# Kernel tuning notes

Hardware: AMD Instinct MI355X
Metric: run time of the kernel (lower is better)

Reference implementation:

```python
import jax, jax.numpy as jnp
import numpy as np

D_MODEL = 512
N_HEADS = 8
HEAD_DIM = D_MODEL // N_HEADS


def setup_inputs() -> dict:
    key = jax.random.key(0)
    ks = jax.random.split(key, 9)
    B, S = 2, 2048
    s = 1.0 / np.sqrt(D_MODEL)
    return {
        "x": jax.random.normal(ks[0], (B, S, D_MODEL), dtype=jnp.float32),
        "wq": jax.random.uniform(ks[1], (D_MODEL, D_MODEL), jnp.float32, -s, s),
        "bq": jax.random.uniform(ks[2], (D_MODEL,), jnp.float32, -s, s),
        "wk": jax.random.uniform(ks[3], (D_MODEL, D_MODEL), jnp.float32, -s, s),
        "bk": jax.random.uniform(ks[4], (D_MODEL,), jnp.float32, -s, s),
        "wv": jax.random.uniform(ks[5], (D_MODEL, D_MODEL), jnp.float32, -s, s),
        "bv": jax.random.uniform(ks[6], (D_MODEL,), jnp.float32, -s, s),
        "wo": jax.random.uniform(ks[7], (D_MODEL, D_MODEL), jnp.float32, -s, s),
        "bo": jax.random.uniform(ks[8], (D_MODEL,), jnp.float32, -s, s),
    }


def reference(x, wq, bq, wk, bk, wv, bv, wo, bo):
    B, S, _ = x.shape
    # Linear layers (torch Linear: y = x @ W.T + b)
    q = x @ wq.T + bq
    k = x @ wk.T + bk
    v = x @ wv.T + bv
    # (B, H, S, Dh)
    def heads(t):
        return t.reshape(B, S, N_HEADS, HEAD_DIM).transpose(0, 2, 1, 3)
    q, k, v = heads(q), heads(k), heads(v)
    scale = 1.0 / np.sqrt(HEAD_DIM)
    scores = jnp.einsum("bhqd,bhkd->bhqk", q, k) * scale
    attn = jax.nn.softmax(scores, axis=-1)
    out = jnp.einsum("bhqk,bhkd->bhqd", attn, v)
    out = out.transpose(0, 2, 1, 3).reshape(B, S, D_MODEL)
    return out @ wo.T + bo
```

## Files before the change

kernel.cpp:

```cpp
#include <hip/hip_runtime.h>
#include <hip/hip_bf16.h>
#include <stdint.h>

typedef unsigned short u16;
typedef __attribute__((ext_vector_type(8))) short short8;
typedef __attribute__((ext_vector_type(4))) float f32x4;
typedef __attribute__((ext_vector_type(4))) unsigned int u32x4;

#define AS1 __attribute__((address_space(1)))
#define AS3 __attribute__((address_space(3)))

__device__ __forceinline__ u16 f2bf(float f) {
    uint32_t u = __float_as_uint(f);
    u += 0x7fffu + ((u >> 16) & 1u);
    return (u16)(u >> 16);
}

__device__ __forceinline__ uint32_t cvtpk(float a, float b) {
    uint32_t r;
    asm("v_cvt_pk_bf16_f32 %0, %1, %2" : "=v"(r) : "v"(a), "v"(b));
    return r;
}

__global__ __launch_bounds__(256) void cvt_kernel(
    const float* __restrict__ x, const float* __restrict__ wq,
    const float* __restrict__ wk, const float* __restrict__ wv,
    const float* __restrict__ wo, u16* __restrict__ dst)
{
    long e = ((long)blockIdx.x * 256 + threadIdx.x) * 8;
    const float* src; long off;
    if (e < 2097152L)      { src = x;  off = e; }
    else if (e < 2359296L) { src = wq; off = e - 2097152L; }
    else if (e < 2621440L) { src = wk; off = e - 2359296L; }
    else if (e < 2883584L) { src = wv; off = e - 2621440L; }
    else                   { src = wo; off = e - 2883584L; }
    float4 a = *(const float4*)(src + off);
    float4 b = *(const float4*)(src + off + 4);
    short8 v;
    v[0] = (short)f2bf(a.x); v[1] = (short)f2bf(a.y);
    v[2] = (short)f2bf(a.z); v[3] = (short)f2bf(a.w);
    v[4] = (short)f2bf(b.x); v[5] = (short)f2bf(b.y);
    v[6] = (short)f2bf(b.z); v[7] = (short)f2bf(b.w);
    *(short8*)(dst + e) = v;
}

__device__ __forceinline__ void gemm_core(
    const u16* __restrict__ A, const u16* __restrict__ Bm,
    int row0, int col0, u16* aSh, u16* bSh, int tid, f32x4 (&acc)[4][4])
{
    const int lane = tid & 63, w = tid >> 6;
    const int lg = lane >> 4, lj = lane & 15;
    const int wr = w >> 1, wc = w & 1;

    for (int ks = 0; ks < 8; ++ks) {
        const int k0 = ks * 64;
#pragma unroll
        for (int rd = 0; rd < 4; ++rd) {
            int t16 = rd * 256 + tid;
            int r = t16 >> 3, p = t16 & 7;
            int l = p ^ (r & 7);
            __builtin_amdgcn_global_load_lds(
                (const AS1 void*)(A + (size_t)(row0 + r) * 512 + k0 + l * 8),
                (AS3 void*)(aSh + t16 * 8), 16, 0, 0);
            __builtin_amdgcn_global_load_lds(
                (const AS1 void*)(Bm + (size_t)(col0 + r) * 512 + k0 + l * 8),
                (AS3 void*)(bSh + t16 * 8), 16, 0, 0);
        }
        __syncthreads();
#pragma unroll
        for (int kt = 0; kt < 2; ++kt) {
            short8 af[4], bf[4];
#pragma unroll
            for (int it = 0; it < 4; ++it) {
                int rowa = wr * 64 + it * 16 + lj;
                int c = kt * 4 + lg;
                af[it] = *(const short8*)((const char*)aSh + rowa * 128 + ((c ^ (rowa & 7)) << 4));
            }
#pragma unroll
            for (int jt = 0; jt < 4; ++jt) {
                int rowb = wc * 64 + jt * 16 + lj;
                int c = kt * 4 + lg;
                bf[jt] = *(const short8*)((const char*)bSh + rowb * 128 + ((c ^ (rowb & 7)) << 4));
            }
#pragma unroll
            for (int it = 0; it < 4; ++it)
#pragma unroll
                for (int jt = 0; jt < 4; ++jt)
                    acc[it][jt] = __builtin_amdgcn_mfma_f32_16x16x32_bf16(af[it], bf[jt], acc[it][jt], 0, 0, 0);
        }
        __syncthreads();
    }
}

__global__ __launch_bounds__(256) void gemm_qkv(
    const u16* __restrict__ xb, const u16* __restrict__ wqb, const u16* __restrict__ wvb,
    const float* __restrict__ bq, const float* __restrict__ bk, const float* __restrict__ bv,
    u16* __restrict__ Qb, u16* __restrict__ Kb, u16* __restrict__ Vtb)
{
    __shared__ u16 aSh[128 * 64];
    __shared__ u16 bSh[128 * 64];
    const int tid = threadIdx.x;
    const int lane = tid & 63, w = tid >> 6;
    const int lg = lane >> 4, lj = lane & 15;
    const int wr = w >> 1, wc = w & 1;
    const int id = blockIdx.x;

    f32x4 acc[4][4] = {};

    if (id < 256) {
        const int row0 = (id >> 3) * 128, col0 = (id & 7) * 128;
        gemm_core(xb, wqb, row0, col0, aSh, bSh, tid, acc);
#pragma unroll
        for (int jt = 0; jt < 4; ++jt) {
            int o = col0 + wc * 64 + jt * 16 + lj;
            float bias = (o < 512) ? bq[o] : bk[o - 512];
            float sc = (o < 512) ? 0.18033688011112042f : 1.0f;
            u16* base = (o < 512) ? Qb : Kb;
            int h = (o >> 6) & 7, d = o & 63;
#pragma unroll
            for (int it = 0; it < 4; ++it)
#pragma unroll
                for (int r = 0; r < 4; ++r) {
                    int n = row0 + wr * 64 + it * 16 + lg * 4 + r;
                    int b = n >> 11, s = n & 2047;
                    base[(size_t)(((b << 3) + h) * 2048 + s) * 64 + d] = f2bf((acc[it][jt][r] + bias) * sc);
                }
        }
    } else {
        const int idx = id - 256;
        const int row0 = (idx >> 5) * 128, col0 = (idx & 31) * 128;
        gemm_core(wvb, xb, row0, col0, aSh, bSh, tid, acc);
#pragma unroll
        for (int it = 0; it < 4; ++it)
#pragma unroll
            for (int r = 0; r < 4; ++r) {
                int orow = row0 + wr * 64 + it * 16 + lg * 4 + r;
                float bias = bv[orow];
#pragma unroll
                for (int jt = 0; jt < 4; ++jt) {
                    int n = col0 + wc * 64 + jt * 16 + lj;
                    Vtb[(size_t)orow * 4096 + n] = f2bf(acc[it][jt][r] + bias);
                }
            }
    }
}

__global__ __launch_bounds__(256) void gemm_out(
    const u16* __restrict__ A, const u16* __restrict__ Bm,
    const float* __restrict__ bias0, float* __restrict__ of32)
{
    __shared__ u16 aSh[128 * 64];
    __shared__ u16 bSh[128 * 64];
    const int tid = threadIdx.x;
    const int lane = tid & 63, w = tid >> 6;
    const int lg = lane >> 4, lj = lane & 15;
    const int wr = w >> 1, wc = w & 1;
    const int row0 = blockIdx.y * 128, col0 = blockIdx.x * 128;

    f32x4 acc[4][4] = {};
    gemm_core(A, Bm, row0, col0, aSh, bSh, tid, acc);

#pragma unroll
    for (int jt = 0; jt < 4; ++jt) {
        int o = col0 + wc * 64 + jt * 16 + lj;
        float bias = bias0[o];
#pragma unroll
        for (int it = 0; it < 4; ++it)
#pragma unroll
            for (int r = 0; r < 4; ++r) {
                int n = row0 + wr * 64 + it * 16 + lg * 4 + r;
                of32[(size_t)n * 512 + o] = acc[it][jt][r] + bias;
            }
    }
}

__global__ __launch_bounds__(256, 4) void attn_kernel(
    const u16* __restrict__ Qb, const u16* __restrict__ Kb,
    const u16* __restrict__ Vtb, float* __restrict__ accP, float* __restrict__ lP)
{
    __shared__ u16 kvSh[2][2][32 * 64];
    const int tid = threadIdx.x;
    const int lane = tid & 63, w = tid >> 6;
    const int lg = lane >> 4, lj = lane & 15;
    const int bh = blockIdx.x, b = bh >> 3, h = bh & 7;
    const int z = blockIdx.z;
    const u16* Qh = Qb + (size_t)bh * 2048 * 64;
    const u16* Kh = Kb + (size_t)bh * 2048 * 64;
    const u16* Vh = Vtb + (size_t)h * 64 * 4096 + b * 2048;
    const int q0 = blockIdx.y * 128 + w * 32;
    const int kvbase = z * 512;

    int koff[2][2];
#pragma unroll
    for (int kt = 0; kt < 2; ++kt)
#pragma unroll
        for (int jf = 0; jf < 2; ++jf) {
            int row = 8 * (lj >> 2) + 4 * jf + (lj & 3);
            int sk = (row & 3) ^ (((row >> 3) & 3) << 1);
            koff[kt][jf] = row * 128 + ((((kt * 4 + lg) ^ sk)) << 4);
        }
    int voff[4];
#pragma unroll
    for (int jd = 0; jd < 4; ++jd) {
        int row = jd * 16 + lj;
        voff[jd] = 4096 + row * 64 + ((lg ^ ((row >> 1) & 3)) << 4);
    }

    {
    }
    int r_ = tid >> 3, p_ = tid & 7;
    int sk_ = (r_ & 3) ^ (((r_ >> 3) & 3) << 1);
    const u16* Ks = Kh + (size_t)(kvbase + r_) * 64 + (p_ ^ sk_) * 8;
    int rv_ = tid >> 2, pv_ = tid & 3;
    const u16* Vs = Vh + (size_t)rv_ * 4096 + kvbase + (pv_ ^ ((rv_ >> 1) & 3)) * 8;
    u16* kd0 = kvSh[0][0] + tid * 8;
    u16* vd0 = kvSh[0][1] + tid * 8;

#define STAGE(KD, VD) do {                                                    \
    __builtin_amdgcn_global_load_lds((const AS1 void*)Ks, (AS3 void*)(KD), 16, 0, 0); \
    __builtin_amdgcn_global_load_lds((const AS1 void*)Vs, (AS3 void*)(VD), 16, 0, 0); \
    Ks += 2048; Vs += 32; } while (0)

    short8 qf[2][2];
#pragma unroll
    for (int g = 0; g < 2; ++g)
#pragma unroll
        for (int kt = 0; kt < 2; ++kt)
            qf[g][kt] = *(const short8*)(Qh + (size_t)(q0 + g * 16 + lj) * 64 + kt * 32 + lg * 8);

    const short8 vone = {0x3F80, 0x3F80, 0x3F80, 0x3F80, 0x3F80, 0x3F80, 0x3F80, 0x3F80};
    f32x4 accO[2][4] = {};
    f32x4 accO5[2] = {};

    auto COMPUTE = [&](int ofs) {
        const char* base = (const char*)kvSh + ofs;
        f32x4 sf[2][2] = {};
#pragma unroll
        for (int kt = 0; kt < 2; ++kt) {
            short8 kf0 = *(const short8*)(base + koff[kt][0]);
            short8 kf1 = *(const short8*)(base + koff[kt][1]);
            sf[0][0] = __builtin_amdgcn_mfma_f32_16x16x32_bf16(kf0, qf[0][kt], sf[0][0], 0, 0, 0);
            sf[0][1] = __builtin_amdgcn_mfma_f32_16x16x32_bf16(kf1, qf[0][kt], sf[0][1], 0, 0, 0);
            sf[1][0] = __builtin_amdgcn_mfma_f32_16x16x32_bf16(kf0, qf[1][kt], sf[1][0], 0, 0, 0);
            sf[1][1] = __builtin_amdgcn_mfma_f32_16x16x32_bf16(kf1, qf[1][kt], sf[1][1], 0, 0, 0);
        }
        u32x4 t0, t1;
        t0[0] = cvtpk(exp2f(sf[0][0][0]), exp2f(sf[0][0][1]));
        t0[1] = cvtpk(exp2f(sf[0][0][2]), exp2f(sf[0][0][3]));
        t0[2] = cvtpk(exp2f(sf[0][1][0]), exp2f(sf[0][1][1]));
        t0[3] = cvtpk(exp2f(sf[0][1][2]), exp2f(sf[0][1][3]));
        t1[0] = cvtpk(exp2f(sf[1][0][0]), exp2f(sf[1][0][1]));
        t1[1] = cvtpk(exp2f(sf[1][0][2]), exp2f(sf[1][0][3]));
        t1[2] = cvtpk(exp2f(sf[1][1][0]), exp2f(sf[1][1][1]));
        t1[3] = cvtpk(exp2f(sf[1][1][2]), exp2f(sf[1][1][3]));
        short8 pa0 = __builtin_bit_cast(short8, t0);
        short8 pa1 = __builtin_bit_cast(short8, t1);
        accO5[0] = __builtin_amdgcn_mfma_f32_16x16x32_bf16(pa0, vone, accO5[0], 0, 0, 0);
        accO5[1] = __builtin_amdgcn_mfma_f32_16x16x32_bf16(pa1, vone, accO5[1], 0, 0, 0);
#pragma unroll
        for (int jd = 0; jd < 4; ++jd) {
            short8 vf = *(const short8*)(base + voff[jd]);
            accO[0][jd] = __builtin_amdgcn_mfma_f32_16x16x32_bf16(pa0, vf, accO[0][jd], 0, 0, 0);
            accO[1][jd] = __builtin_amdgcn_mfma_f32_16x16x32_bf16(pa1, vf, accO[1][jd], 0, 0, 0);
        }
    };

    STAGE(kd0, vd0);
    __syncthreads();
    for (int it = 0; it < 8; ++it) {
        STAGE(kd0 + 4096, vd0 + 4096);
        COMPUTE(0);
        __syncthreads();
        if (it < 7) STAGE(kd0, vd0);
        COMPUTE(8192);
        __syncthreads();
    }
#undef STAGE

    float* accW = accP + (size_t)z * 2097152;
#pragma unroll
    for (int g = 0; g < 2; ++g)
#pragma unroll
        for (int r = 0; r < 4; ++r) {
            int q = q0 + g * 16 + lg * 4 + r;
            int s = b * 2048 + q;
#pragma unroll
            for (int jd = 0; jd < 4; ++jd)
                accW[(size_t)s * 512 + h * 64 + jd * 16 + lj] = accO[g][jd][r];
            if (lj == 0) lP[(z * 16 + bh) * 2048 + q] = accO5[g][r];
        }
}

__global__ __launch_bounds__(256) void combine_kernel(
    const float* __restrict__ accP, const float* __restrict__ lP, u16* __restrict__ Ob)
{
    int gid = blockIdx.x * 256 + threadIdx.x;
    int row = gid >> 6, cb = (gid & 63) * 8;
    int b = row >> 11, q = row & 2047;
    int h = (gid & 63) >> 3;
    int bh = b * 8 + h;
    float l = 0.0f;
#pragma unroll
    for (int z = 0; z < 4; ++z) l += lP[z * 32768 + bh * 2048 + q];
    float inv = 1.0f / l;
    float s[8] = {};
#pragma unroll
    for (int z = 0; z < 4; ++z) {
        const float* a = accP + (size_t)z * 2097152 + (size_t)row * 512 + cb;
        float4 x0 = *(const float4*)a, x1 = *(const float4*)(a + 4);
        s[0] += x0.x; s[1] += x0.y; s[2] += x0.z; s[3] += x0.w;
        s[4] += x1.x; s[5] += x1.y; s[6] += x1.z; s[7] += x1.w;
    }
    short8 o;
#pragma unroll
    for (int j = 0; j < 8; ++j) o[j] = (short)f2bf(s[j] * inv);
    *(short8*)(Ob + (size_t)gid * 8) = o;
}

extern "C" void kernel_launch(void* const* d_in, const int* in_sizes, int n_in,
                              void* d_out, int out_size, void* d_ws, size_t ws_size,
                              hipStream_t stream)
{
    const float* x  = (const float*)d_in[0];
    const float* wq = (const float*)d_in[1];
    const float* bq = (const float*)d_in[2];
    const float* wk = (const float*)d_in[3];
    const float* bk = (const float*)d_in[4];
    const float* wv = (const float*)d_in[5];
    const float* bv = (const float*)d_in[6];
    const float* wo = (const float*)d_in[7];
    const float* bo = (const float*)d_in[8];

    u16* w16 = (u16*)d_ws;
    u16* xb  = w16;
    u16* wqb = w16 + 2097152;
    u16* wvb = w16 + 2621440;
    u16* wob = w16 + 2883584;
    u16* Qb  = w16 + 3145728;
    u16* Kb  = w16 + 5242880;
    u16* Vtb = w16 + 7340032;
    u16* Ob  = w16 + 9437184;
    float* accPf = (float*)(w16 + 11534336);
    float* lPf   = accPf + 8388608;

    cvt_kernel<<<1536, 256, 0, stream>>>(x, wq, wk, wv, wo, w16);
    gemm_qkv<<<384, 256, 0, stream>>>(xb, wqb, wvb, bq, bk, bv, Qb, Kb, Vtb);
    attn_kernel<<<dim3(16, 16, 4), 256, 0, stream>>>(Qb, Kb, Vtb, accPf, lPf);
    combine_kernel<<<1024, 256, 0, stream>>>(accPf, lPf, Ob);
    gemm_out<<<dim3(4, 32), 256, 0, stream>>>(Ob, wob, bo, (float*)d_out);
}
```

Measured before the change: 72.72 us.

## Fuse split-KV combine into attention via last-block counter; use 128x64 GEMM tiles

Removes the separate combine kernel. Each attention block now increments a per-(head, query-tile) atomic counter, and the last of the four KV-split blocks reduces the partial accumulators and normalisers into bf16 output. The counter is zeroed inside the conversion kernel. The V projection and output projection GEMMs switch to a new 128x64 tile core, raising block counts from 128 to 256 for the output GEMM and from 128 to 256 for the V part, to fill more CUs. The trade-offs are extra atomics and thread fences, plus a serial reduction tail on the last-arriving blocks.

```diff
diff --git a/kernel.cpp b/kernel.cpp
--- a/kernel.cpp
+++ b/kernel.cpp
@@ -25,8 +25,9 @@
 __global__ __launch_bounds__(256) void cvt_kernel(
     const float* __restrict__ x, const float* __restrict__ wq,
     const float* __restrict__ wk, const float* __restrict__ wv,
-    const float* __restrict__ wo, u16* __restrict__ dst)
-{
+    const float* __restrict__ wo, u16* __restrict__ dst, int* __restrict__ cnt)
+{
+    if (blockIdx.x == 0) cnt[threadIdx.x] = 0;
     long e = ((long)blockIdx.x * 256 + threadIdx.x) * 8;
     const float* src; long off;
     if (e < 2097152L)      { src = x;  off = e; }
@@ -92,6 +93,60 @@
     }
 }
 
+__device__ __forceinline__ void gemm_core64(
+    const u16* __restrict__ A, const u16* __restrict__ Bm,
+    int row0, int col0, u16* aSh, u16* bSh, int tid, f32x4 (&acc)[4][2])
+{
+    const int lane = tid & 63, w = tid >> 6;
+    const int lg = lane >> 4, lj = lane & 15;
+    const int wr = w >> 1, wc = w & 1;
+
+    for (int ks = 0; ks < 8; ++ks) {
+        const int k0 = ks * 64;
+#pragma unroll
+        for (int rd = 0; rd < 4; ++rd) {
+            int t16 = rd * 256 + tid;
+            int r = t16 >> 3, p = t16 & 7;
+            int l = p ^ (r & 7);
+            __builtin_amdgcn_global_load_lds(
+                (const AS1 void*)(A + (size_t)(row0 + r) * 512 + k0 + l * 8),
+                (AS3 void*)(aSh + t16 * 8), 16, 0, 0);
+        }
+#pragma unroll
+        for (int rd = 0; rd < 2; ++rd) {
+            int t16 = rd * 256 + tid;
+            int r = t16 >> 3, p = t16 & 7;
+            int l = p ^ (r & 7);
+            __builtin_amdgcn_global_load_lds(
+                (const AS1 void*)(Bm + (size_t)(col0 + r) * 512 + k0 + l * 8),
+                (AS3 void*)(bSh + t16 * 8), 16, 0, 0);
+        }
+        __syncthreads();
+#pragma unroll
+        for (int kt = 0; kt < 2; ++kt) {
+            short8 af[4], bf[2];
+#pragma unroll
+            for (int it = 0; it < 4; ++it) {
+                int rowa = wr * 64 + it * 16 + lj;
+                int c = kt * 4 + lg;
+                af[it] = *(const short8*)((const char*)aSh + rowa * 128 + ((c ^ (rowa & 7)) << 4));
+            }
+#pragma unroll
+            for (int jt = 0; jt < 2; ++jt) {
+                int rowb = wc * 32 + jt * 16 + lj;
+                int c = kt * 4 + lg;
+                bf[jt] = *(const short8*)((const char*)bSh + rowb * 128 + ((c ^ (rowb & 7)) << 4));
+            }
+#pragma unroll
+            for (int it = 0; it < 4; ++it)
+#pragma unroll
+                for (int jt = 0; jt < 2; ++jt)
+                    acc[it][jt] = __builtin_amdgcn_mfma_f32_16x16x32_bf16(af[it], bf[jt], acc[it][jt], 0, 0, 0);
+        }
+        __syncthreads();
+    }
+}
+
 __global__ __launch_bounds__(256) void gemm_qkv(
     const u16* __restrict__ xb, const u16* __restrict__ wqb, const u16* __restrict__ wvb,
     const float* __restrict__ bq, const float* __restrict__ bk, const float* __restrict__ bv,
@@ -105,9 +160,8 @@
     const int wr = w >> 1, wc = w & 1;
     const int id = blockIdx.x;
 
-    f32x4 acc[4][4] = {};
-
     if (id < 256) {
+        f32x4 acc[4][4] = {};
         const int row0 = (id >> 3) * 128, col0 = (id & 7) * 128;
         gemm_core(xb, wqb, row0, col0, aSh, bSh, tid, acc);
 #pragma unroll
@@ -127,9 +181,10 @@
                 }
         }
     } else {
+        f32x4 acc[4][2] = {};
         const int idx = id - 256;
-        const int row0 = (idx >> 5) * 128, col0 = (idx & 31) * 128;
-        gemm_core(wvb, xb, row0, col0, aSh, bSh, tid, acc);
+        const int row0 = (idx >> 6) * 128, col0 = (idx & 63) * 64;
+        gemm_core64(wvb, xb, row0, col0, aSh, bSh, tid, acc);
 #pragma unroll
         for (int it = 0; it < 4; ++it)
 #pragma unroll
@@ -137,8 +192,8 @@
                 int orow = row0 + wr * 64 + it * 16 + lg * 4 + r;
                 float bias = bv[orow];
 #pragma unroll
-                for (int jt = 0; jt < 4; ++jt) {
-                    int n = col0 + wc * 64 + jt * 16 + lj;
+                for (int jt = 0; jt < 2; ++jt) {
+                    int n = col0 + wc * 32 + jt * 16 + lj;
                     Vtb[(size_t)orow * 4096 + n] = f2bf(acc[it][jt][r] + bias);
                 }
             }
@@ -150,19 +205,20 @@
     const float* __restrict__ bias0, float* __restrict__ of32)
 {
     __shared__ u16 aSh[128 * 64];
-    __shared__ u16 bSh[128 * 64];
+    __shared__ u16 bSh[64 * 64];
     const int tid = threadIdx.x;
     const int lane = tid & 63, w = tid >> 6;
     const int lg = lane >> 4, lj = lane & 15;
     const int wr = w >> 1, wc = w & 1;
-    const int row0 = blockIdx.y * 128, col0 = blockIdx.x * 128;
-
-    f32x4 acc[4][4] = {};
-    gemm_core(A, Bm, row0, col0, aSh, bSh, tid, acc);
-
-#pragma unroll
-    for (int jt = 0; jt < 4; ++jt) {
-        int o = col0 + wc * 64 + jt * 16 + lj;
+    const int id = blockIdx.x;
+    const int row0 = (id >> 3) * 128, col0 = (id & 7) * 64;
+
+    f32x4 acc[4][2] = {};
+    gemm_core64(A, Bm, row0, col0, aSh, bSh, tid, acc);
+
+#pragma unroll
+    for (int jt = 0; jt < 2; ++jt) {
+        int o = col0 + wc * 32 + jt * 16 + lj;
         float bias = bias0[o];
 #pragma unroll
         for (int it = 0; it < 4; ++it)
@@ -176,7 +232,8 @@
 
 __global__ __launch_bounds__(256, 4) void attn_kernel(
     const u16* __restrict__ Qb, const u16* __restrict__ Kb,
-    const u16* __restrict__ Vtb, float* __restrict__ accP, float* __restrict__ lP)
+    const u16* __restrict__ Vtb, float* __restrict__ accP, float* __restrict__ lP,
+    u16* __restrict__ Ob, int* __restrict__ cnt)
 {
     __shared__ u16 kvSh[2][2][32 * 64];
     const int tid = threadIdx.x;
@@ -206,8 +263,6 @@
         voff[jd] = 4096 + row * 64 + ((lg ^ ((row >> 1) & 3)) << 4);
     }
 
-    {
-    }
     int r_ = tid >> 3, p_ = tid & 7;
     int sk_ = (r_ & 3) ^ (((r_ >> 3) & 3) << 1);
     const u16* Ks = Kh + (size_t)(kvbase + r_) * 64 + (p_ ^ sk_) * 8;
@@ -289,32 +344,41 @@
                 accW[(size_t)s * 512 + h * 64 + jd * 16 + lj] = accO[g][jd][r];
             if (lj == 0) lP[(z * 16 + bh) * 2048 + q] = accO5[g][r];
         }
-}
-
-__global__ __launch_bounds__(256) void combine_kernel(
-    const float* __restrict__ accP, const float* __restrict__ lP, u16* __restrict__ Ob)
-{
-    int gid = blockIdx.x * 256 + threadIdx.x;
-    int row = gid >> 6, cb = (gid & 63) * 8;
-    int b = row >> 11, q = row & 2047;
-    int h = (gid & 63) >> 3;
-    int bh = b * 8 + h;
-    float l = 0.0f;
-#pragma unroll
-    for (int z = 0; z < 4; ++z) l += lP[z * 32768 + bh * 2048 + q];
-    float inv = 1.0f / l;
-    float s[8] = {};
-#pragma unroll
-    for (int z = 0; z < 4; ++z) {
-        const float* a = accP + (size_t)z * 2097152 + (size_t)row * 512 + cb;
-        float4 x0 = *(const float4*)a, x1 = *(const float4*)(a + 4);
-        s[0] += x0.x; s[1] += x0.y; s[2] += x0.z; s[3] += x0.w;
-        s[4] += x1.x; s[5] += x1.y; s[6] += x1.z; s[7] += x1.w;
-    }
-    short8 o;
-#pragma unroll
-    for (int j = 0; j < 8; ++j) o[j] = (short)f2bf(s[j] * inv);
-    *(short8*)(Ob + (size_t)gid * 8) = o;
+
+    __threadfence();
+    __shared__ int amLast;
+    if (tid == 0)
+        amLast = (atomicAdd(&cnt[bh * 16 + blockIdx.y], 1) == 3);
+    __syncthreads();
+    if (amLast) {
+        __threadfence();
+        int qi = tid >> 1, dh = (tid & 1) * 32;
+        int q = blockIdx.y * 128 + qi;
+        int s = b * 2048 + q;
+        float l = 0.0f;
+#pragma unroll
+        for (int zz = 0; zz < 4; ++zz) l += lP[(zz * 16 + bh) * 2048 + q];
+        float inv = 1.0f / l;
+        float sa[32] = {};
+#pragma unroll
+        for (int zz = 0; zz < 4; ++zz) {
+            const float* a = accP + (size_t)zz * 2097152 + (size_t)s * 512 + h * 64 + dh;
+#pragma unroll
+            for (int j = 0; j < 8; ++j) {
+                float4 v4 = *(const float4*)(a + j * 4);
+                sa[j * 4 + 0] += v4.x; sa[j * 4 + 1] += v4.y;
+                sa[j * 4 + 2] += v4.z; sa[j * 4 + 3] += v4.w;
+            }
+        }
+        u16* ob = Ob + (size_t)s * 512 + h * 64 + dh;
+#pragma unroll
+        for (int j = 0; j < 4; ++j) {
+            short8 o8;
+#pragma unroll
+            for (int k = 0; k < 8; ++k) o8[k] = (short)f2bf(sa[j * 8 + k] * inv);
+            *(short8*)(ob + j * 8) = o8;
+        }
+    }
 }
 
 extern "C" void kernel_launch(void* const* d_in, const int* in_sizes, int n_in,
@@ -342,10 +406,10 @@
     u16* Ob  = w16 + 9437184;
     float* accPf = (float*)(w16 + 11534336);
     float* lPf   = accPf + 8388608;
-
-    cvt_kernel<<<1536, 256, 0, stream>>>(x, wq, wk, wv, wo, w16);
-    gemm_qkv<<<384, 256, 0, stream>>>(xb, wqb, wvb, bq, bk, bv, Qb, Kb, Vtb);
-    attn_kernel<<<dim3(16, 16, 4), 256, 0, stream>>>(Qb, Kb, Vtb, accPf, lPf);
-    combine_kernel<<<1024, 256, 0, stream>>>(accPf, lPf, Ob);
-    gemm_out<<<dim3(4, 32), 256, 0, stream>>>(Ob, wob, bo, (float*)d_out);
-}
+    int*   cnt   = (int*)(lPf + 131072);
+
+    cvt_kernel<<<1536, 256, 0, stream>>>(x, wq, wk, wv, wo, w16, cnt);
+    gemm_qkv<<<512, 256, 0, stream>>>(xb, wqb, wvb, bq, bk, bv, Qb, Kb, Vtb);
+    attn_kernel<<<dim3(16, 16, 4), 256, 0, stream>>>(Qb, Kb, Vtb, accPf, lPf, Ob, cnt);
+    gemm_out<<<256, 256, 0, stream>>>(Ob, wob, bo, (float*)d_out);
+}
```

Result: slower. 213.8 us (+193.9%).
